# Optimization experiments

Hardware: AMD Instinct MI355X
Metric: run time of the kernel (lower is better)

Reference implementation:

```python
import jax, jax.numpy as jnp
import numpy as np

NUM_GROUPS = 32
NUM_HEADS = 8
EPS = 1e-5


def setup_inputs() -> dict:
    key = jax.random.key(0)
    ks = jax.random.split(key, 3)
    C = 512
    x = jax.random.normal(ks[0], (4, C, 48, 48), dtype=jnp.float32)
    gamma = jnp.ones((C,), jnp.float32)
    beta = jnp.zeros((C,), jnp.float32)
    w_qkv = jax.random.normal(ks[1], (C, 3 * C), jnp.float32) * (1.0 / np.sqrt(C))
    b_qkv = jnp.zeros((3 * C,), jnp.float32)
    w_proj = jax.random.normal(ks[2], (C, C), jnp.float32) * (1.0 / np.sqrt(C))
    b_proj = jnp.zeros((C,), jnp.float32)
    return {"x": x, "gamma": gamma, "beta": beta, "w_qkv": w_qkv,
            "b_qkv": b_qkv, "w_proj": w_proj, "b_proj": b_proj}


def group_norm(x, gamma, beta):
    # x: (b, c, h, w); 32 groups over channel dim
    b, c, h, w = x.shape
    xg = x.reshape(b, NUM_GROUPS, c // NUM_GROUPS, h, w)
    mu = jnp.mean(xg, axis=(2, 3, 4), keepdims=True)
    var = jnp.var(xg, axis=(2, 3, 4), keepdims=True)
    xn = ((xg - mu) * jax.lax.rsqrt(var + EPS)).reshape(b, c, h, w)
    return xn * gamma[None, :, None, None] + beta[None, :, None, None]


def reference(x, gamma, beta, w_qkv, b_qkv, w_proj, b_proj):
    b, c, h, w = x.shape
    hd = c // NUM_HEADS
    scale = hd ** -0.5
    xn = group_norm(x, gamma, beta)
    x_flat = xn.reshape(b, c, h * w).transpose(0, 2, 1)          # (b, s, c)
    qkv = x_flat @ w_qkv + b_qkv                                  # (b, s, 3c)
    q, k, v = jnp.split(qkv, 3, axis=-1)
    s = h * w
    # (b, heads, s, hd)
    q = q.reshape(b, s, NUM_HEADS, hd).transpose(0, 2, 1, 3)
    k = k.reshape(b, s, NUM_HEADS, hd).transpose(0, 2, 1, 3)
    v = v.reshape(b, s, NUM_HEADS, hd).transpose(0, 2, 1, 3)
    attn = jnp.einsum('bhqd,bhkd->bhqk', q, k) * scale            # (b, h, s, s)
    attn = jax.nn.softmax(attn, axis=-1)
    out = jnp.einsum('bhqk,bhkd->bhqd', attn, v)                  # (b, h, s, hd)
    out = out.transpose(0, 2, 1, 3).reshape(b, s, c)
    out = out @ w_proj + b_proj                                   # (b, s, c)
    return x + out.transpose(0, 2, 1).reshape(b, c, h, w)
```

## Files before the change

kernel.cpp:

```cpp
#include <hip/hip_runtime.h>
#include <hip/hip_bf16.h>
#include <stdint.h>

#define S_LEN 2304
#define C_DIM 512
#define NH 8
#define HD 64

typedef __attribute__((ext_vector_type(8))) __bf16 bf16x8;
typedef __attribute__((ext_vector_type(4))) float f32x4;
typedef __attribute__((ext_vector_type(16))) float f32x16;
typedef __attribute__((ext_vector_type(8))) unsigned short u16x8;
typedef __attribute__((ext_vector_type(4))) unsigned short u16x4;
typedef __attribute__((ext_vector_type(4))) unsigned int u32x4;

__device__ __forceinline__ unsigned short bf16u(float f) {
  __hip_bfloat16 h = __float2bfloat16(f);
  return __builtin_bit_cast(unsigned short, h);
}

__device__ __forceinline__ void load_lds16(const void* g, void* l) {
  __builtin_amdgcn_global_load_lds(
      (const __attribute__((address_space(1))) void*)g,
      (__attribute__((address_space(3))) void*)l, 16, 0, 0);
}

__device__ __forceinline__ float max3f(float a, float b, float c) {
  float d;
  asm("v_max3_f32 %0, %1, %2, %3" : "=v"(d) : "v"(a), "v"(b), "v"(c));
  return d;
}

__global__ __launch_bounds__(256) void gn_stats_kernel(const float* __restrict__ x,
                                                       float* __restrict__ stats) {
  const int bg = blockIdx.x;
  const float4* src = (const float4*)(x + (size_t)bg * 36864);
  float s = 0.f, s2 = 0.f;
#pragma unroll
  for (int i = 0; i < 36; ++i) {
    float4 v = src[i * 256 + threadIdx.x];
    s += v.x + v.y + v.z + v.w;
    s2 += v.x * v.x + v.y * v.y + v.z * v.z + v.w * v.w;
  }
#pragma unroll
  for (int off = 1; off < 64; off <<= 1) {
    s += __shfl_xor(s, off);
    s2 += __shfl_xor(s2, off);
  }
  __shared__ float red[8];
  const int wid = threadIdx.x >> 6;
  if ((threadIdx.x & 63) == 0) { red[wid] = s; red[wid + 4] = s2; }
  __syncthreads();
  if (threadIdx.x == 0) {
    float S = red[0] + red[1] + red[2] + red[3];
    float S2 = red[4] + red[5] + red[6] + red[7];
    float mu = S * (1.f / 36864.f);
    float var = S2 * (1.f / 36864.f) - mu * mu;
    stats[bg * 2] = mu;
    stats[bg * 2 + 1] = rsqrtf(var + 1e-5f);
  }
}

__global__ __launch_bounds__(256) void gn_norm_t_kernel(
    const float* __restrict__ x, const float* __restrict__ gamma,
    const float* __restrict__ beta, const float* __restrict__ stats,
    unsigned short* __restrict__ xn) {
  __shared__ float tile[64][68];
  const int s0 = blockIdx.x * 64, c0 = blockIdx.y * 64, b = blockIdx.z;
  const int tid = threadIdx.x;
  {
    const int cl = tid >> 2, sc = (tid & 3) * 16;
    const float* src = x + ((size_t)b * C_DIM + c0 + cl) * S_LEN + s0 + sc;
#pragma unroll
    for (int i = 0; i < 4; ++i)
      *(float4*)&tile[cl][sc + i * 4] = *(const float4*)(src + i * 4);
  }
  __syncthreads();
  const int sl = tid >> 2, cc = (tid & 3) * 16;
  const int g = (c0 + cc) >> 4;
  const float mu = stats[((size_t)b * 32 + g) * 2];
  const float rs = stats[((size_t)b * 32 + g) * 2 + 1];
  u16x8 o0, o1;
#pragma unroll
  for (int j = 0; j < 8; ++j) {
    const int c = c0 + cc + j;
    o0[j] = bf16u((tile[cc + j][sl] - mu) * rs * gamma[c] + beta[c]);
  }
#pragma unroll
  for (int j = 0; j < 8; ++j) {
    const int c = c0 + cc + 8 + j;
    o1[j] = bf16u((tile[cc + 8 + j][sl] - mu) * rs * gamma[c] + beta[c]);
  }
  unsigned short* dst = xn + ((size_t)b * S_LEN + s0 + sl) * C_DIM + c0 + cc;
  *(u16x8*)dst = o0;
  *(u16x8*)(dst + 8) = o1;
}

__global__ __launch_bounds__(256) void wt_kernel(const float* __restrict__ w,
                                                 unsigned short* __restrict__ wT,
                                                 int N, int K) {
  __shared__ float tile[64][68];
  const int n0 = blockIdx.x * 64, k0 = blockIdx.y * 64;
  const int tid = threadIdx.x;
  {
    const int kl = tid >> 2, nc = (tid & 3) * 16;
    const float* src = w + (size_t)(k0 + kl) * N + n0 + nc;
#pragma unroll
    for (int i = 0; i < 4; ++i)
      *(float4*)&tile[kl][nc + i * 4] = *(const float4*)(src + i * 4);
  }
  __syncthreads();
  const int nl = tid >> 2, kc = (tid & 3) * 16;
  u16x8 o0, o1;
#pragma unroll
  for (int j = 0; j < 8; ++j) o0[j] = bf16u(tile[kc + j][nl]);
#pragma unroll
  for (int j = 0; j < 8; ++j) o1[j] = bf16u(tile[kc + 8 + j][nl]);
  unsigned short* dst = wT + (size_t)(n0 + nl) * K + k0 + kc;
  *(u16x8*)dst = o0;
  *(u16x8*)(dst + 8) = o1;
}

__device__ __forceinline__ void gemm128_core(const unsigned short* __restrict__ A,
                                             const unsigned short* __restrict__ B,
                                             int K, int m0, int n0, short* lds_a,
                                             short* lds_b, f32x4 (&acc)[4][4]) {
  const int tid = threadIdx.x;
  const int lane = tid & 63, wid = tid >> 6;
  const int wr = wid >> 1, wc = wid & 1;
  const f32x4 fzero = {0.f, 0.f, 0.f, 0.f};
#pragma unroll
  for (int i = 0; i < 4; ++i)
#pragma unroll
    for (int j = 0; j < 4; ++j) acc[i][j] = fzero;
  const int lrow = lane >> 3;
  const int lcol = (lane & 7) * 8;
  for (int kt = 0; kt < K; kt += 64) {
#pragma unroll
    for (int i = 0; i < 4; ++i) {
      const int r0 = (wid * 4 + i) * 8;
      load_lds16((const void*)(A + (size_t)(m0 + r0 + lrow) * K + kt + lcol), lds_a + r0 * 64);
      load_lds16((const void*)(B + (size_t)(n0 + r0 + lrow) * K + kt + lcol), lds_b + r0 * 64);
    }
    __syncthreads();
#pragma unroll
    for (int ks = 0; ks < 2; ++ks) {
      bf16x8 af[4], bfr[4];
#pragma unroll
      for (int mf = 0; mf < 4; ++mf)
        af[mf] = *(const bf16x8*)(lds_a + ((wr * 64 + mf * 16 + (lane & 15)) * 64 +
                                           ks * 32 + (lane >> 4) * 8));
#pragma unroll
      for (int nf = 0; nf < 4; ++nf)
        bfr[nf] = *(const bf16x8*)(lds_b + ((wc * 64 + nf * 16 + (lane & 15)) * 64 +
                                            ks * 32 + (lane >> 4) * 8));
#pragma unroll
      for (int mf = 0; mf < 4; ++mf)
#pragma unroll
        for (int nf = 0; nf < 4; ++nf)
          acc[mf][nf] =
              __builtin_amdgcn_mfma_f32_16x16x32_bf16(af[mf], bfr[nf], acc[mf][nf], 0, 0, 0);
    }
    __syncthreads();
  }
}

__global__ __launch_bounds__(256) void qkv_gemm_kernel(
    const unsigned short* __restrict__ xn, const unsigned short* __restrict__ wT,
    const float* __restrict__ bq, unsigned short* __restrict__ Qb,
    unsigned short* __restrict__ Kb, unsigned short* __restrict__ Vt) {
  __shared__ short lds_a[128 * 64];
  __shared__ short lds_b[128 * 64];
  const int b = blockIdx.z;
  const int m0 = blockIdx.x * 128, n0 = blockIdx.y * 128;
  f32x4 acc[4][4];
  gemm128_core(xn + (size_t)b * S_LEN * C_DIM, wT, C_DIM, m0, n0, lds_a, lds_b, acc);
  const int lane = threadIdx.x & 63, wid = threadIdx.x >> 6;
  const int wr = wid >> 1, wc = wid & 1;
#pragma unroll
  for (int mf = 0; mf < 4; ++mf) {
#pragma unroll
    for (int nf = 0; nf < 4; ++nf) {
      const int n = n0 + wc * 64 + nf * 16 + (lane & 15);
      const int part = n >> 9;
      const int h = (n >> 6) & 7;
      const int d = n & 63;
      const float bias = bq[n];
      const int m = m0 + wr * 64 + mf * 16 + (lane >> 4) * 4;
      if (part == 2) {
        u16x4 pk;
#pragma unroll
        for (int r = 0; r < 4; ++r) pk[r] = bf16u(acc[mf][nf][r] + bias);
        *(u16x4*)(Vt + ((size_t)(b * NH + h) * HD + d) * S_LEN + m) = pk;
      } else {
        unsigned short* dst = part == 0 ? Qb : Kb;
        const float sc = part == 0 ? 0.18033688011112042f : 1.0f;
#pragma unroll
        for (int r = 0; r < 4; ++r)
          dst[((size_t)(b * NH + h) * S_LEN + m + r) * HD + d] =
              bf16u((acc[mf][nf][r] + bias) * sc);
      }
    }
  }
}

#define QBLK 96
__global__ __launch_bounds__(192) void attn_kernel(const unsigned short* __restrict__ Q,
                                                   const unsigned short* __restrict__ K,
                                                   const unsigned short* __restrict__ Vt,
                                                   unsigned short* __restrict__ O) {
  __shared__ __align__(16) char smem[49152];
  const int tid = threadIdx.x;
  const int w = tid >> 6, l = tid & 63;
  const int l31 = l & 31, hi = l >> 5;
  const int bh = blockIdx.y, b = bh >> 3, h = bh & 7;
  const int q0 = blockIdx.x * QBLK;

  const char* gQ = (const char*)Q + (size_t)bh * S_LEN * 128;
  const char* gK = (const char*)K + (size_t)bh * S_LEN * 128;
  const char* gV = (const char*)Vt + (size_t)bh * HD * (S_LEN * 2);

  bf16x8 qf[4];
  {
    const char* qp = gQ + (size_t)(q0 + w * 32 + l31) * 128 + hi * 16;
#pragma unroll
    for (int d4 = 0; d4 < 4; ++d4) qf[d4] = *(const bf16x8*)(qp + d4 * 32);
  }
  asm volatile("" : "+v"(qf[0]), "+v"(qf[1]), "+v"(qf[2]), "+v"(qf[3]));

  const char* kvp[6];
  unsigned kvadv[6];
  bool kvok[6];
#pragma unroll
  for (int i = 0; i < 6; ++i) {
    const int c = i * 192 + tid;
    kvok[i] = (c < 1024);
    if (c < 512) {
      const int r = c >> 3, ch = c & 7;
      kvp[i] = gK + (size_t)r * 128 + ((ch ^ (r & 7)) << 4);
      kvadv[i] = 64 * 128;
    } else {
      const int c2 = c & 511;
      const int dd = c2 >> 3, ch = c2 & 7;
      kvp[i] = gV + (size_t)dd * (S_LEN * 2) + ((ch ^ (dd & 7)) << 4);
      kvadv[i] = 128;
    }
  }

  auto stage_kv = [&](char* nreg) {
#pragma unroll
    for (int i = 0; i < 6; ++i) {
      if (kvok[i]) {
        load_lds16((const void*)kvp[i], nreg + (i * 192 + w * 64) * 16);
        kvp[i] += kvadv[i];
      }
    }
  };

  stage_kv(smem);
  stage_kv(smem + 16384);

  const u16x8 onesu = {0x3F80, 0x3F80, 0x3F80, 0x3F80, 0x3F80, 0x3F80, 0x3F80, 0x3F80};
  const bf16x8 onesf = __builtin_bit_cast(bf16x8, onesu);

  float m_run = -1e30f;
  f32x16 oac0, oac1, lacc;
#pragma unroll
  for (int i = 0; i < 16; ++i) { oac0[i] = 0.f; oac1[i] = 0.f; lacc[i] = 0.f; }

  int cur = 0;
  for (int kt = 0; kt < 36; ++kt) {
    char* region = smem + cur * 16384;
    if (kt <= 33) {
      int nxt = cur + 2; if (nxt >= 3) nxt -= 3;
      stage_kv(smem + nxt * 16384);
      if (w == 0) asm volatile("s_waitcnt vmcnt(12)" ::: "memory");
      else        asm volatile("s_waitcnt vmcnt(10)" ::: "memory");
    } else if (kt == 34) {
      if (w == 0) asm volatile("s_waitcnt vmcnt(6)" ::: "memory");
      else        asm volatile("s_waitcnt vmcnt(5)" ::: "memory");
    } else {
      asm volatile("s_waitcnt vmcnt(0)" ::: "memory");
    }
    __builtin_amdgcn_s_barrier();

    const char* kreg = region;
    const char* vreg = region + 8192;
#pragma unroll
    for (int sub = 0; sub < 2; ++sub) {
      f32x16 st;
#pragma unroll
      for (int i = 0; i < 16; ++i) st[i] = 0.f;
      const int krow = sub * 32 + l31;
      const int ksw = krow & 7;
#pragma unroll
      for (int d4 = 0; d4 < 4; ++d4) {
        bf16x8 kf = *(const bf16x8*)(kreg + krow * 128 + (((d4 * 2 + hi) ^ ksw) << 4));
        st = __builtin_amdgcn_mfma_f32_32x32x16_bf16(kf, qf[d4], st, 0, 0, 0);
      }
      float m0 = max3f(st[0], st[1], st[2]);
      float m1 = max3f(st[3], st[4], st[5]);
      float m2 = max3f(st[6], st[7], st[8]);
      float m3 = max3f(st[9], st[10], st[11]);
      float m4 = max3f(st[12], st[13], st[14]);
      float mt = max3f(m0, m1, st[15]);
      float mb = max3f(m2, m3, m4);
      mt = fmaxf(mt, mb);
      {
        float mo = mt;
        asm volatile("v_permlane32_swap_b32 %0, %1" : "+v"(mt), "+v"(mo));
        mt = fmaxf(mt, mo);
      }
      if (__any((mt - m_run) > 8.f)) {
        const float mnew = fmaxf(m_run, mt);
        const float corr = exp2f(m_run - mnew);
#pragma unroll
        for (int i = 0; i < 16; ++i) { oac0[i] *= corr; oac1[i] *= corr; lacc[i] *= corr; }
        m_run = mnew;
      }
      float p[16];
#pragma unroll
      for (int i = 0; i < 16; ++i) p[i] = exp2f(st[i] - m_run);
      unsigned int wv[8];
#pragma unroll
      for (int j = 0; j < 8; ++j)
        asm("v_cvt_pk_bf16_f32 %0, %1, %2" : "=v"(wv[j]) : "v"(p[2 * j]), "v"(p[2 * j + 1]));
      asm volatile("v_permlane32_swap_b32 %0, %1" : "+v"(wv[0]), "+v"(wv[2]));
      asm volatile("v_permlane32_swap_b32 %0, %1" : "+v"(wv[1]), "+v"(wv[3]));
      asm volatile("v_permlane32_swap_b32 %0, %1" : "+v"(wv[4]), "+v"(wv[6]));
      asm volatile("v_permlane32_swap_b32 %0, %1" : "+v"(wv[5]), "+v"(wv[7]));
      u32x4 pw0 = {wv[0], wv[1], wv[2], wv[3]};
      u32x4 pw1 = {wv[4], wv[5], wv[6], wv[7]};
      bf16x8 pf0 = __builtin_bit_cast(bf16x8, pw0);
      bf16x8 pf1 = __builtin_bit_cast(bf16x8, pw1);
      lacc = __builtin_amdgcn_mfma_f32_32x32x16_bf16(onesf, pf0, lacc, 0, 0, 0);
      lacc = __builtin_amdgcn_mfma_f32_32x32x16_bf16(onesf, pf1, lacc, 0, 0, 0);
      {
        const int vrow = l31;
        const int vsw = vrow & 7;
        bf16x8 vf0 = *(const bf16x8*)(vreg + vrow * 128 + (((sub * 4 + 0 + hi) ^ vsw) << 4));
        oac0 = __builtin_amdgcn_mfma_f32_32x32x16_bf16(vf0, pf0, oac0, 0, 0, 0);
        bf16x8 vf1 = *(const bf16x8*)(vreg + vrow * 128 + (((sub * 4 + 2 + hi) ^ vsw) << 4));
        oac0 = __builtin_amdgcn_mfma_f32_32x32x16_bf16(vf1, pf1, oac0, 0, 0, 0);
      }
      {
        const int vrow = 32 + l31;
        const int vsw = vrow & 7;
        bf16x8 vf0 = *(const bf16x8*)(vreg + vrow * 128 + (((sub * 4 + 0 + hi) ^ vsw) << 4));
        oac1 = __builtin_amdgcn_mfma_f32_32x32x16_bf16(vf0, pf0, oac1, 0, 0, 0);
        bf16x8 vf1 = *(const bf16x8*)(vreg + vrow * 128 + (((sub * 4 + 2 + hi) ^ vsw) << 4));
        oac1 = __builtin_amdgcn_mfma_f32_32x32x16_bf16(vf1, pf1, oac1, 0, 0, 0);
      }
    }
    __builtin_amdgcn_s_barrier();
    ++cur; if (cur >= 3) cur -= 3;
  }

  __syncthreads();
  const float inv = 1.f / lacc[0];
  unsigned short* ob = (unsigned short*)smem;
  const int qrow = w * 32 + l31;
#pragma unroll
  for (int g = 0; g < 4; ++g) {
    u16x4 pk;
#pragma unroll
    for (int r = 0; r < 4; ++r) pk[r] = bf16u(oac0[g * 4 + r] * inv);
    *(u16x4*)(ob + qrow * 72 + (g * 8 + hi * 4)) = pk;
  }
#pragma unroll
  for (int g = 0; g < 4; ++g) {
    u16x4 pk;
#pragma unroll
    for (int r = 0; r < 4; ++r) pk[r] = bf16u(oac1[g * 4 + r] * inv);
    *(u16x4*)(ob + qrow * 72 + (32 + g * 8 + hi * 4)) = pk;
  }
  __syncthreads();
#pragma unroll
  for (int i = 0; i < 4; ++i) {
    const int c = i * 192 + tid;
    const int row = c >> 3, c8 = (c & 7) * 8;
    u16x8 v = *(const u16x8*)(ob + row * 72 + c8);
    *(u16x8*)(O + ((size_t)b * S_LEN + q0 + row) * C_DIM + h * HD + c8) = v;
  }
}

__global__ __launch_bounds__(256) void proj_gemm_kernel(
    const unsigned short* __restrict__ wT, const unsigned short* __restrict__ ao,
    const float* __restrict__ bp, const float* __restrict__ x, float* __restrict__ out) {
  __shared__ short lds_a[128 * 64];
  __shared__ short lds_b[128 * 64];
  const int b = blockIdx.z;
  const int m0 = blockIdx.x * 128, n0 = blockIdx.y * 128;
  f32x4 acc[4][4];
  gemm128_core(wT, ao + (size_t)b * S_LEN * C_DIM, C_DIM, m0, n0, lds_a, lds_b, acc);
  const int lane = threadIdx.x & 63, wid = threadIdx.x >> 6;
  const int wr = wid >> 1, wc = wid & 1;
#pragma unroll
  for (int mf = 0; mf < 4; ++mf) {
#pragma unroll
    for (int nf = 0; nf < 4; ++nf) {
      const int n = n0 + wc * 64 + nf * 16 + (lane & 15);
#pragma unroll
      for (int r = 0; r < 4; ++r) {
        const int m = m0 + wr * 64 + mf * 16 + (lane >> 4) * 4 + r;
        const size_t idx = ((size_t)b * C_DIM + m) * S_LEN + n;
        out[idx] = x[idx] + acc[mf][nf][r] + bp[m];
      }
    }
  }
}

extern "C" void kernel_launch(void* const* d_in, const int* in_sizes, int n_in,
                              void* d_out, int out_size, void* d_ws, size_t ws_size,
                              hipStream_t stream) {
  const float* x = (const float*)d_in[0];
  const float* gamma = (const float*)d_in[1];
  const float* beta = (const float*)d_in[2];
  const float* w_qkv = (const float*)d_in[3];
  const float* b_qkv = (const float*)d_in[4];
  const float* w_proj = (const float*)d_in[5];
  const float* b_proj = (const float*)d_in[6];
  float* out = (float*)d_out;

  char* ws = (char*)d_ws;
  float* stats = (float*)ws;
  unsigned short* xn = (unsigned short*)(ws + 1024);
  unsigned short* wqkvT = (unsigned short*)(ws + 9438208);
  unsigned short* wprojT = (unsigned short*)(ws + 11011072);
  unsigned short* Qb = (unsigned short*)(ws + 11535360);
  unsigned short* Kb = (unsigned short*)(ws + 20972544);
  unsigned short* Vt = (unsigned short*)(ws + 30409728);
  unsigned short* ao = (unsigned short*)(ws + 39846912);

  hipLaunchKernelGGL(gn_stats_kernel, dim3(128), dim3(256), 0, stream, x, stats);
  hipLaunchKernelGGL(wt_kernel, dim3(24, 8), dim3(256), 0, stream, w_qkv, wqkvT, 3 * C_DIM, C_DIM);
  hipLaunchKernelGGL(wt_kernel, dim3(8, 8), dim3(256), 0, stream, w_proj, wprojT, C_DIM, C_DIM);
  hipLaunchKernelGGL(gn_norm_t_kernel, dim3(36, 8, 4), dim3(256), 0, stream, x, gamma, beta, stats, xn);
  hipLaunchKernelGGL(qkv_gemm_kernel, dim3(18, 12, 4), dim3(256), 0, stream, xn, wqkvT, b_qkv, Qb, Kb, Vt);
  hipLaunchKernelGGL(attn_kernel, dim3(24, 32), dim3(192), 0, stream, Qb, Kb, Vt, ao);
  hipLaunchKernelGGL(proj_gemm_kernel, dim3(4, 18, 4), dim3(256), 0, stream, wprojT, ao, b_proj, x, out);
}
```

Measured before the change: 194.3 us.

## Stage Q through swizzled LDS and switch KV pipeline to double buffering

Q is now loaded into LDS with async global_load_lds and a swizzled layout alongside the first KV tile, then read into registers, replacing direct per-thread global loads. The KV ring changes from triple to double buffering, which cuts LDS from 48KB to 44KB and removes the modulo-3 buffer index. The first QK MFMA also starts from a constant zero vector instead of a zeroed accumulator. The shallower prefetch may expose more global latency per tile, while the smaller LDS footprint may allow more blocks per CU.

```diff
diff --git a/kernel.cpp b/kernel.cpp
--- a/kernel.cpp
+++ b/kernel.cpp
@@ -209,7 +209,7 @@
                                                    const unsigned short* __restrict__ K,
                                                    const unsigned short* __restrict__ Vt,
                                                    unsigned short* __restrict__ O) {
-  __shared__ __align__(16) char smem[49152];
+  __shared__ __align__(16) char smem[45056];
   const int tid = threadIdx.x;
   const int w = tid >> 6, l = tid & 63;
   const int l31 = l & 31, hi = l >> 5;
@@ -219,14 +219,6 @@
   const char* gQ = (const char*)Q + (size_t)bh * S_LEN * 128;
   const char* gK = (const char*)K + (size_t)bh * S_LEN * 128;
   const char* gV = (const char*)Vt + (size_t)bh * HD * (S_LEN * 2);
-
-  bf16x8 qf[4];
-  {
-    const char* qp = gQ + (size_t)(q0 + w * 32 + l31) * 128 + hi * 16;
-#pragma unroll
-    for (int d4 = 0; d4 < 4; ++d4) qf[d4] = *(const bf16x8*)(qp + d4 * 32);
-  }
-  asm volatile("" : "+v"(qf[0]), "+v"(qf[1]), "+v"(qf[2]), "+v"(qf[3]));
 
   const char* kvp[6];
   unsigned kvadv[6];
@@ -257,26 +249,43 @@
     }
   };
 
-  stage_kv(smem);
-  stage_kv(smem + 16384);
+#pragma unroll
+  for (int i = 0; i < 4; ++i) {
+    const int c0 = i * 192 + w * 64;
+    const int c = c0 + l;
+    const int r = c >> 3, ch = c & 7;
+    load_lds16((const void*)(gQ + (size_t)(q0 + r) * 128 + ((ch ^ (r & 7)) << 4)),
+               smem + c0 * 16);
+  }
+  stage_kv(smem + 12288);
+  if (w == 0) asm volatile("s_waitcnt vmcnt(6)" ::: "memory");
+  else        asm volatile("s_waitcnt vmcnt(5)" ::: "memory");
+  __builtin_amdgcn_s_barrier();
+
+  bf16x8 qf[4];
+  {
+    const int qrow = w * 32 + l31;
+    const int qsw = qrow & 7;
+#pragma unroll
+    for (int d4 = 0; d4 < 4; ++d4)
+      qf[d4] = *(const bf16x8*)(smem + qrow * 128 + (((d4 * 2 + hi) ^ qsw) << 4));
+  }
 
   const u16x8 onesu = {0x3F80, 0x3F80, 0x3F80, 0x3F80, 0x3F80, 0x3F80, 0x3F80, 0x3F80};
   const bf16x8 onesf = __builtin_bit_cast(bf16x8, onesu);
+  f32x16 z16;
+#pragma unroll
+  for (int i = 0; i < 16; ++i) z16[i] = 0.f;
 
   float m_run = -1e30f;
   f32x16 oac0, oac1, lacc;
 #pragma unroll
   for (int i = 0; i < 16; ++i) { oac0[i] = 0.f; oac1[i] = 0.f; lacc[i] = 0.f; }
 
-  int cur = 0;
   for (int kt = 0; kt < 36; ++kt) {
-    char* region = smem + cur * 16384;
-    if (kt <= 33) {
-      int nxt = cur + 2; if (nxt >= 3) nxt -= 3;
-      stage_kv(smem + nxt * 16384);
-      if (w == 0) asm volatile("s_waitcnt vmcnt(12)" ::: "memory");
-      else        asm volatile("s_waitcnt vmcnt(10)" ::: "memory");
-    } else if (kt == 34) {
+    char* region = smem + 12288 + ((kt & 1) << 14);
+    if (kt < 35) {
+      stage_kv(smem + 12288 + (((kt + 1) & 1) << 14));
       if (w == 0) asm volatile("s_waitcnt vmcnt(6)" ::: "memory");
       else        asm volatile("s_waitcnt vmcnt(5)" ::: "memory");
     } else {
@@ -288,13 +297,15 @@
     const char* vreg = region + 8192;
 #pragma unroll
     for (int sub = 0; sub < 2; ++sub) {
-      f32x16 st;
-#pragma unroll
-      for (int i = 0; i < 16; ++i) st[i] = 0.f;
       const int krow = sub * 32 + l31;
       const int ksw = krow & 7;
-#pragma unroll
-      for (int d4 = 0; d4 < 4; ++d4) {
+      f32x16 st;
+      {
+        bf16x8 kf = *(const bf16x8*)(kreg + krow * 128 + (((0 + hi) ^ ksw) << 4));
+        st = __builtin_amdgcn_mfma_f32_32x32x16_bf16(kf, qf[0], z16, 0, 0, 0);
+      }
+#pragma unroll
+      for (int d4 = 1; d4 < 4; ++d4) {
         bf16x8 kf = *(const bf16x8*)(kreg + krow * 128 + (((d4 * 2 + hi) ^ ksw) << 4));
         st = __builtin_amdgcn_mfma_f32_32x32x16_bf16(kf, qf[d4], st, 0, 0, 0);
       }
@@ -353,7 +364,6 @@
       }
     }
     __builtin_amdgcn_s_barrier();
-    ++cur; if (cur >= 3) cur -= 3;
   }
 
   __syncthreads();
```

After: 194.7 us. About the same (+0.2%).
